# Optimization experiments

Hardware: AMD Instinct MI355X
Metric: run time of the kernel (lower is better)

## Reference

```python
import jax, jax.numpy as jnp
import numpy as np
import math

B, L, DM = 2, 2048, 1536
H, FD = 12, 16          # num_heads, feature_dim
DV = DM // H            # head_dim = 128
D2 = FD * FD            # expanded Taylor feature dim = 256
CHUNK = 128
EPS = 1e-12
LN_EPS = 1e-5


def setup_inputs() -> dict:
    key = jax.random.key(0)
    ks = jax.random.split(key, 5)
    s = lambda fan_in: 1.0 / math.sqrt(fan_in)
    return {
        "hidden_states": jax.random.normal(ks[0], (B, L, DM), jnp.float32),
        "Wq": jax.random.normal(ks[1], (DM, H * FD), jnp.float32) * s(DM),
        "Wk": jax.random.normal(ks[2], (DM, H * FD), jnp.float32) * s(DM),
        "Wv": jax.random.normal(ks[3], (DM, H * DV), jnp.float32) * s(DM),
        "Wo": jax.random.normal(ks[4], (H * DV, DM), jnp.float32) * s(H * DV),
        "ln_q_g": jnp.ones((H * FD,), jnp.float32),
        "ln_q_b": jnp.zeros((H * FD,), jnp.float32),
        "ln_k_g": jnp.ones((H * FD,), jnp.float32),
        "ln_k_b": jnp.zeros((H * FD,), jnp.float32),
    }


def _layernorm(x, g, b):
    mu = x.mean(-1, keepdims=True)
    var = ((x - mu) ** 2).mean(-1, keepdims=True)
    return (x - mu) * jax.lax.rsqrt(var + LN_EPS) * g + b


def _taylor_exp(x):
    # x: (b, h, l, d) -> flattened outer product / sqrt(d): (b, h, l, d*d)
    x2 = x[..., :, None] * x[..., None, :]
    return x2.reshape(*x.shape[:-1], -1) / math.sqrt(FD)


def _rebased_forward(hidden_states, Wq, Wk, Wv, Wo, ln_q_g, ln_q_b, ln_k_g, ln_k_b):
    b, l, _ = hidden_states.shape
    q = _layernorm(hidden_states @ Wq, ln_q_g, ln_q_b)
    k = _layernorm(hidden_states @ Wk, ln_k_g, ln_k_b)
    v = hidden_states @ Wv
    # (b, l, h*d) -> (b, h, l, d)
    q = q.reshape(b, l, H, FD).transpose(0, 2, 1, 3)
    k = k.reshape(b, l, H, FD).transpose(0, 2, 1, 3)
    v = v.reshape(b, l, H, DV).transpose(0, 2, 1, 3)
    q2 = _taylor_exp(q)  # (b, h, l, D2)
    k2 = _taylor_exp(k)

    nC = l // CHUNK
    # chunk-major layout for scan: (nC, b, h, C, .)
    q2c = q2.reshape(b, H, nC, CHUNK, D2).transpose(2, 0, 1, 3, 4)
    k2c = k2.reshape(b, H, nC, CHUNK, D2).transpose(2, 0, 1, 3, 4)
    vc = v.reshape(b, H, nC, CHUNK, DV).transpose(2, 0, 1, 3, 4)
    mask = jnp.tril(jnp.ones((CHUNK, CHUNK), q2.dtype))  # causal within chunk

    S0 = jnp.zeros((b, H, D2, DV), q2.dtype)  # running sum of k2^T v
    z0 = jnp.zeros((b, H, D2), q2.dtype)      # running sum of k2

    def step(carry, inp):
        S, z = carry
        qc, kc, vcur = inp
        A = jnp.einsum("bhcd,bhed->bhce", qc, kc) * mask  # intra-chunk scores
        num = jnp.einsum("bhcd,bhdv->bhcv", qc, S) + jnp.einsum("bhce,bhev->bhcv", A, vcur)
        den = jnp.einsum("bhcd,bhd->bhc", qc, z) + A.sum(-1)
        o = num / (den[..., None] + EPS)
        S = S + jnp.einsum("bhed,bhev->bhdv", kc, vcur)
        z = z + kc.sum(2)
        return (S, z), o

    _, o = jax.lax.scan(step, (S0, z0), (q2c, k2c, vc))
    # (nC, b, h, C, dv) -> (b, l, h*dv)
    o = o.transpose(1, 2, 0, 3, 4).reshape(b, H, l, DV).transpose(0, 2, 1, 3).reshape(b, l, H * DV)
    return o @ Wo


def reference(hidden_states, Wq, Wk, Wv, Wo, ln_q_g, ln_q_b, ln_k_g, ln_k_b):
    return _rebased_forward(hidden_states, Wq, Wk, Wv, Wo, ln_q_g, ln_q_b, ln_k_g, ln_k_b)
```

## Files before the change

kernel.cpp:

```cpp
#include <hip/hip_runtime.h>
#include <hip/hip_bf16.h>
#include <math.h>

#define Bc   2
#define Lc   2048
#define DMc  1536
#define Hc   12
#define FDc  16
#define DVc  128
#define D2c  256
#define CHK  128
#define NCH  16
#define ROWS (Bc*Lc)
#define HFD  (Hc*FDc)
#define HDV  (Hc*DVc)
#define NQK  (2*HFD)
#define NPRJ (NQK + HDV)

typedef __bf16 bf16x8 __attribute__((ext_vector_type(8)));
typedef float f32x4 __attribute__((ext_vector_type(4)));

__device__ __forceinline__ float bf2f(unsigned short u) {
    return __uint_as_float(((unsigned int)u) << 16);
}
__device__ __forceinline__ unsigned short f2bf(float v) {
    unsigned int u = __float_as_uint(v);
    unsigned int r = (u + 0x7FFFu + ((u >> 16) & 1u)) >> 16;
    return (unsigned short)r;
}
__device__ __forceinline__ unsigned int pack2(unsigned short a, unsigned short b) {
    return (unsigned int)a | ((unsigned int)b << 16);
}
__device__ __forceinline__ float ldin(const void* p, size_t i, int isf32) {
    return isf32 ? ((const float*)p)[i] : bf2f(((const unsigned short*)p)[i]);
}

#define GLL16(g, l) __builtin_amdgcn_global_load_lds( \
    (const __attribute__((address_space(1))) unsigned int*)(g), \
    (__attribute__((address_space(3))) unsigned int*)(l), 16, 0, 0)

__global__ void probe_dtype(const unsigned short* __restrict__ hs, int* __restrict__ flag) {
    const int tid = threadIdx.x;
    int sane = 0;
    for (int i = tid; i < 1024; i += 256) {
        unsigned short b = hs[2 * i];
        int e = (b >> 7) & 0xFF;
        if (e >= 97 && e <= 157) sane++;
    }
    __shared__ int tot;
    if (tid == 0) tot = 0;
    __syncthreads();
    atomicAdd(&tot, sane);
    __syncthreads();
    if (tid == 0) *flag = (tot >= 614) ? 0 : 1;
}

__global__ __launch_bounds__(256) void conv_bf16(const void* __restrict__ X,
                                                 unsigned short* __restrict__ Y,
                                                 int n4, const int* __restrict__ flagp) {
    const int f = *flagp;
    int i = blockIdx.x * 256 + threadIdx.x;
    if (i >= n4) return;
    if (f) {
        float4 x = ((const float4*)X)[i];
        ushort4 y;
        y.x = f2bf(x.x); y.y = f2bf(x.y); y.z = f2bf(x.z); y.w = f2bf(x.w);
        ((ushort4*)Y)[i] = y;
    } else {
        ((ushort4*)Y)[i] = ((const ushort4*)X)[i];
    }
}

__global__ __launch_bounds__(256) void convT_bf16(const void* __restrict__ W,
                                                  unsigned short* __restrict__ Wt,
                                                  int rows, int cols,
                                                  const int* __restrict__ flagp) {
    const int f = *flagp;
    __shared__ float tile[64][65];
    const int t = threadIdx.x;
    const int bx = blockIdx.x * 64;
    const int by = blockIdx.y * 64;
#pragma unroll
    for (int u = 0; u < 16; u++) {
        int idx = t + u * 256;
        int r = idx >> 6, c = idx & 63;
        tile[r][c] = ldin(W, (size_t)(by + r) * cols + bx + c, f);
    }
    __syncthreads();
#pragma unroll
    for (int u = 0; u < 16; u++) {
        int idx = t + u * 256;
        int r = idx >> 6, c = idx & 63;
        Wt[(size_t)(bx + r) * rows + by + c] = f2bf(tile[c][r]);
    }
}

__global__ __launch_bounds__(512) void gemm_mfma_bt(const unsigned short* __restrict__ A,
                                                    const unsigned short* __restrict__ Bt,
                                                    void* __restrict__ C,
                                                    int M, int N, int K,
                                                    int ldc,
                                                    int cMode, const int* __restrict__ flagp,
                                                    unsigned short* __restrict__ vTout) {
    const int f = *flagp;
    __shared__ __align__(16) unsigned char smem[32768];
    unsigned short* As = (unsigned short*)smem;
    unsigned short* Bsu = As + 8192;
    f32x4* scr4 = (f32x4*)smem;

    const int tid = threadIdx.x;
    const int wave = tid >> 6, lane = tid & 63;
    const int kgrp = wave >> 2;
    const int w4 = wave & 3;
    const int row0 = blockIdx.y * 128, col0 = blockIdx.x * 128;
    const int wrow = (w4 >> 1) * 64, wcol = (w4 & 1) * 64;
    const int mlane = lane & 15, quad = lane >> 4;
    const int kHalf = K >> 1;

    const unsigned short* Ab = A + (size_t)row0 * K + (size_t)kgrp * kHalf;
    const unsigned short* Bb = Bt + (size_t)col0 * K + (size_t)kgrp * kHalf;
    const int t256 = tid & 255;
    const int r0 = t256 >> 2;
    const int kc = (t256 & 3) * 8;
    const size_t off0 = (size_t)r0 * K + kc;
    const size_t off1 = (size_t)(r0 + 64) * K + kc;
    char* AsW = (char*)As + kgrp * 8192 + w4 * 1024;
    char* BsW = (char*)Bsu + kgrp * 8192 + w4 * 1024;
    const int ldsBase = kgrp * 4096;

    f32x4 acc[4][4] = {};

    for (int k0 = 0; k0 < kHalf; k0 += 32) {
        GLL16(Ab + off0 + k0, AsW);
        GLL16(Ab + off1 + k0, AsW + 4096);
        GLL16(Bb + off0 + k0, BsW);
        GLL16(Bb + off1 + k0, BsW + 4096);
        __syncthreads();
        bf16x8 a[4], b[4];
#pragma unroll
        for (int i = 0; i < 4; i++)
            a[i] = *(const bf16x8*)&As[ldsBase + (wrow + i * 16 + mlane) * 32 + quad * 8];
#pragma unroll
        for (int j = 0; j < 4; j++)
            b[j] = *(const bf16x8*)&Bsu[ldsBase + (wcol + j * 16 + mlane) * 32 + quad * 8];
#pragma unroll
        for (int i = 0; i < 4; i++)
#pragma unroll
            for (int j = 0; j < 4; j++)
                acc[i][j] = __builtin_amdgcn_mfma_f32_16x16x32_bf16(a[i], b[j], acc[i][j], 0, 0, 0);
        __syncthreads();
    }

    {
        const int col = (wave & 1) * 64 + lane;
        if (kgrp == 1 && w4 < 2) {
#pragma unroll
            for (int i = 0; i < 4; i++)
#pragma unroll
                for (int j = 0; j < 4; j++)
                    scr4[(i * 4 + j) * 128 + col] = acc[i][j];
        }
        __syncthreads();
        if (kgrp == 0 && w4 < 2) {
#pragma unroll
            for (int i = 0; i < 4; i++)
#pragma unroll
                for (int j = 0; j < 4; j++)
                    acc[i][j] += scr4[(i * 4 + j) * 128 + col];
        }
        __syncthreads();
        if (kgrp == 1 && w4 >= 2) {
#pragma unroll
            for (int i = 0; i < 4; i++)
#pragma unroll
                for (int j = 0; j < 4; j++)
                    scr4[(i * 4 + j) * 128 + col] = acc[i][j];
        }
        __syncthreads();
        if (kgrp == 0 && w4 >= 2) {
#pragma unroll
            for (int i = 0; i < 4; i++)
#pragma unroll
                for (int j = 0; j < 4; j++)
                    acc[i][j] += scr4[(i * 4 + j) * 128 + col];
        }
    }
    if (kgrp != 0) return;

    float* Cf = nullptr;
    unsigned short* Cb16 = nullptr;
    bool doT = false;
    int tOff = 0;
    if (cMode == 0) Cf = (float*)C;
    else if (cMode == 1) Cb16 = (unsigned short*)C;
    else if (cMode == 2) { if (f) Cf = (float*)C; else Cb16 = (unsigned short*)C; }
    else if (cMode == 4) {
        if (col0 < NQK) Cf = (float*)C;
        else { doT = true; tOff = NQK; }
    }
    if (cMode <= 3 && vTout) doT = true;

#pragma unroll
    for (int i = 0; i < 4; i++)
#pragma unroll
        for (int j = 0; j < 4; j++) {
            const int col = col0 + wcol + j * 16 + mlane;
            if (Cf) {
#pragma unroll
                for (int r = 0; r < 4; r++) {
                    const int row = row0 + wrow + i * 16 + quad * 4 + r;
                    Cf[(size_t)row * ldc + col] = acc[i][j][r];
                }
            } else if (Cb16) {
#pragma unroll
                for (int r = 0; r < 4; r++) {
                    const int row = row0 + wrow + i * 16 + quad * 4 + r;
                    Cb16[(size_t)row * ldc + col] = f2bf(acc[i][j][r]);
                }
            }
            if (doT) {
                ushort4 pk;
                pk.x = f2bf(acc[i][j][0]); pk.y = f2bf(acc[i][j][1]);
                pk.z = f2bf(acc[i][j][2]); pk.w = f2bf(acc[i][j][3]);
                *(ushort4*)(vTout + (size_t)(col - tOff) * M + row0 + wrow + i * 16 + quad * 4) = pk;
            }
        }
}

__global__ __launch_bounds__(192) void ln_kernel(const float* __restrict__ qk,
                                                 float* __restrict__ q, float* __restrict__ k,
                                                 const void* __restrict__ gq,
                                                 const void* __restrict__ bq,
                                                 const void* __restrict__ gk,
                                                 const void* __restrict__ bk,
                                                 const int* __restrict__ flagp) {
    const int f = *flagp;
    const int row = blockIdx.x, t = threadIdx.x;
    float vq = qk[(size_t)row * NQK + t];
    float vk = qk[(size_t)row * NQK + HFD + t];
    float s[4] = {vq, vq * vq, vk, vk * vk};
    __shared__ float part[4][3];
    const int w = t >> 6, lane = t & 63;
#pragma unroll
    for (int i = 0; i < 4; i++) {
        float v = s[i];
        for (int off = 32; off; off >>= 1) v += __shfl_down(v, off);
        if (lane == 0) part[i][w] = v;
    }
    __syncthreads();
    float sq  = part[0][0] + part[0][1] + part[0][2];
    float sq2 = part[1][0] + part[1][1] + part[1][2];
    float sk  = part[2][0] + part[2][1] + part[2][2];
    float sk2 = part[3][0] + part[3][1] + part[3][2];
    const float inv = 1.0f / (float)HFD;
    float muq = sq * inv, muk = sk * inv;
    float varq = sq2 * inv - muq * muq;
    float vark = sk2 * inv - muk * muk;
    float oq = (vq - muq) * rsqrtf(varq + 1e-5f) * ldin(gq, t, f) + ldin(bq, t, f);
    float ok = (vk - muk) * rsqrtf(vark + 1e-5f) * ldin(gk, t, f) + ldin(bk, t, f);
    q[(size_t)row * HFD + t] = oq;
    k[(size_t)row * HFD + t] = ok;
}

__global__ __launch_bounds__(256) void state_prefix_mfma(const float* __restrict__ kn,
                                                         const unsigned short* __restrict__ vT,
                                                         unsigned short* __restrict__ St,
                                                         float* __restrict__ zc) {
    const int bx = blockIdx.x;
    const int by = blockIdx.y;
    const int bh = blockIdx.z;
    const int h = bh % Hc, b = bh / Hc;
    const int t0 = bx * 16;
    const int tid = threadIdx.x;
    const int wave = tid >> 6, lane = tid & 63;
    const int mlane = lane & 15, quad = lane >> 4;

    __shared__ __align__(16) float kcs[CHK * FDc];
    __shared__ __align__(16) unsigned short K2t[16 * 136];
    __shared__ __align__(16) unsigned short Vs[64 * 136];
    __shared__ float zp[16][17];
    __shared__ float zpre[16];
    if (tid < 16) zpre[tid] = 0.f;

    f32x4 acc = {};
    const int kr = tid >> 1, khf = tid & 1;
    const int d2l = tid & 15, cg = tid >> 4;
    const int vrow = tid >> 2, vseg = tid & 3;
    const int dvL = wave * 16 + mlane;

    for (int n = 0; n < NCH; n++) {
        const int row0 = b * Lc + n * CHK;
        __syncthreads();
        {
            const float4* src = (const float4*)(kn + (size_t)(row0 + kr) * HFD + h * FDc + khf * 8);
            *(float4*)(kcs + kr * 16 + khf * 8)     = src[0];
            *(float4*)(kcs + kr * 16 + khf * 8 + 4) = src[1];
            const uint4* g = (const uint4*)(vT + (size_t)(h * 128 + by * 64 + vrow) * ROWS + row0 + vseg * 32);
            *(uint4*)(Vs + vrow * 136 + vseg * 32)      = g[0];
            *(uint4*)(Vs + vrow * 136 + vseg * 32 + 8)  = g[1];
            *(uint4*)(Vs + vrow * 136 + vseg * 32 + 16) = g[2];
            *(uint4*)(Vs + vrow * 136 + vseg * 32 + 24) = g[3];
        }
        __syncthreads();
        {
            float zs_ = 0.f;
            unsigned short pk[8];
#pragma unroll
            for (int u = 0; u < 8; u++) {
                int c = cg * 8 + u;
                float p = kcs[c * 16 + bx] * kcs[c * 16 + d2l] * 0.25f;
                zs_ += p;
                pk[u] = f2bf(p);
            }
            uint4 w;
            w.x = pack2(pk[0], pk[1]); w.y = pack2(pk[2], pk[3]);
            w.z = pack2(pk[4], pk[5]); w.w = pack2(pk[6], pk[7]);
            *(uint4*)(K2t + d2l * 136 + cg * 8) = w;
            zp[d2l][cg] = zs_;
        }
        __syncthreads();
        {
            size_t base = (((size_t)(bh * NCH + n) * 16 + bx) * 128) * 16;
            int dv = by * 64 + dvL;
            ushort4 pk;
            pk.x = f2bf(acc[0]); pk.y = f2bf(acc[1]);
            pk.z = f2bf(acc[2]); pk.w = f2bf(acc[3]);
            *(ushort4*)(St + base + (size_t)dv * 16 + quad * 4) = pk;
            if (tid < 16) {
                float s = 0.f;
#pragma unroll
                for (int c = 0; c < 16; c++) s += zp[tid][c];
                if (by == 0)
                    zc[(size_t)(bh * NCH + n) * D2c + t0 + tid] = zpre[tid];
                zpre[tid] += s;
            }
        }
        {
#pragma unroll
            for (int ks = 0; ks < 4; ks++) {
                bf16x8 a = *(const bf16x8*)(K2t + mlane * 136 + ks * 32 + quad * 8);
                bf16x8 bfr = *(const bf16x8*)(Vs + dvL * 136 + ks * 32 + quad * 8);
                acc = __builtin_amdgcn_mfma_f32_16x16x32_bf16(a, bfr, acc, 0, 0, 0);
            }
        }
    }
}

__global__ __launch_bounds__(256) void chunk_out_mfma(const float* __restrict__ qn,
                                                      const float* __restrict__ kn,
                                                      const unsigned short* __restrict__ St,
                                                      const float* __restrict__ z,
                                                      const unsigned short* __restrict__ vT,
                                                      unsigned short* __restrict__ o) {
    const int blk = blockIdx.x;
    const int n = blk & 15, bh = blk >> 4;
    const int h = bh % Hc, b = bh / Hc;
    const int row0 = b * Lc + n * CHK;
    const int tid = threadIdx.x;
    const int wave = tid >> 6, lane = tid & 63;
    const int mlane = lane & 15, quad = lane >> 4;
    const int wrow = (wave >> 1) * 64, wcol = (wave & 1) * 64;

    __shared__ __align__(16) unsigned char lds[61952];
    float* Qs   = (float*)lds;
    float* zs   = (float*)(lds + 8192);
    float* denp = (float*)(lds + 9216);
    float* dinv = (float*)(lds + 10240);
    unsigned char* U = lds + 10752;
    unsigned short* Q2s = (unsigned short*)U;
    unsigned short* Sts = (unsigned short*)(U + 10240);
    unsigned short* Kb  = (unsigned short*)U;
    unsigned short* Qb  = (unsigned short*)(U + 8192);
    unsigned short* At  = (unsigned short*)(U + 16384);
    unsigned short* Vs  = (unsigned short*)U;

    {
        int r = tid >> 1, hf = tid & 1;
        const float4* src = (const float4*)(qn + (size_t)(row0 + r) * HFD + h * FDc + hf * 8);
        *(float4*)(Qs + r * 16 + hf * 8)     = src[0];
        *(float4*)(Qs + r * 16 + hf * 8 + 4) = src[1];
        if (tid < 64)
            ((float4*)zs)[tid] = ((const float4*)(z + ((size_t)bh * NCH + n) * D2c))[tid];
    }
    __syncthreads();

    const int qc = tid >> 1, qhalf = tid & 1;
    float qr[16];
#pragma unroll
    for (int ff = 0; ff < 16; ff++) qr[ff] = Qs[qc * 16 + ff];

    f32x4 acc[4][4] = {};
    float den1 = 0.f;
    const unsigned short* Stb = St + ((size_t)bh * NCH + n) * ((size_t)D2c * DVc);

    for (int k0 = 0; k0 < 256; k0 += 32) {
        {
            unsigned short pk[16];
#pragma unroll
            for (int kk = 0; kk < 16; kk++) {
                int d2 = k0 + qhalf * 16 + kk;
                float val = qr[d2 >> 4] * qr[d2 & 15] * 0.25f;
                den1 += val * zs[d2];
                pk[kk] = f2bf(val);
            }
            uint4 w0, w1;
            w0.x = pack2(pk[0], pk[1]);  w0.y = pack2(pk[2], pk[3]);
            w0.z = pack2(pk[4], pk[5]);  w0.w = pack2(pk[6], pk[7]);
            w1.x = pack2(pk[8], pk[9]);  w1.y = pack2(pk[10], pk[11]);
            w1.z = pack2(pk[12], pk[13]); w1.w = pack2(pk[14], pk[15]);
            *(uint4*)(Q2s + qc * 40 + qhalf * 16) = w0;
            *(uint4*)(Q2s + qc * 40 + qhalf * 16 + 8) = w1;
        }
        {
            int r = tid >> 1, hf = tid & 1;
            const uint4* g = (const uint4*)(Stb + (size_t)((k0 >> 4) + hf) * 2048 + r * 16);
            uint4 d0 = g[0], d1 = g[1];
            *(uint4*)(Sts + r * 40 + hf * 16) = d0;
            *(uint4*)(Sts + r * 40 + hf * 16 + 8) = d1;
        }
        __syncthreads();
        bf16x8 a[4], bfr[4];
#pragma unroll
        for (int i = 0; i < 4; i++)
            a[i] = *(const bf16x8*)(Q2s + (wrow + i * 16 + mlane) * 40 + quad * 8);
#pragma unroll
        for (int j = 0; j < 4; j++)
            bfr[j] = *(const bf16x8*)(Sts + (wcol + j * 16 + mlane) * 40 + quad * 8);
#pragma unroll
        for (int i = 0; i < 4; i++)
#pragma unroll
            for (int j = 0; j < 4; j++)
                acc[i][j] = __builtin_amdgcn_mfma_f32_16x16x32_bf16(a[i], bfr[j], acc[i][j], 0, 0, 0);
        __syncthreads();
    }
    denp[qhalf * 128 + qc] = den1;

    {
        int r = tid >> 1, hf = tid & 1;
        if (hf == 0) {
            unsigned short pq[16], pkk[16];
#pragma unroll
            for (int ff = 0; ff < 16; ff++) pq[ff] = f2bf(Qs[r * 16 + ff]);
            const float* kg = kn + (size_t)(row0 + r) * HFD + h * FDc;
#pragma unroll
            for (int ff = 0; ff < 16; ff++) pkk[ff] = f2bf(kg[ff]);
            uint4 w;
            w.x = pack2(pq[0], pq[1]);  w.y = pack2(pq[2], pq[3]);
            w.z = pack2(pq[4], pq[5]);  w.w = pack2(pq[6], pq[7]);
            *(uint4*)(Qb + r * 32) = w;
            w.x = pack2(pq[8], pq[9]);  w.y = pack2(pq[10], pq[11]);
            w.z = pack2(pq[12], pq[13]); w.w = pack2(pq[14], pq[15]);
            *(uint4*)(Qb + r * 32 + 8) = w;
            w.x = pack2(pkk[0], pkk[1]);  w.y = pack2(pkk[2], pkk[3]);
            w.z = pack2(pkk[4], pkk[5]);  w.w = pack2(pkk[6], pkk[7]);
            *(uint4*)(Kb + r * 32) = w;
            w.x = pack2(pkk[8], pkk[9]);  w.y = pack2(pkk[10], pkk[11]);
            w.z = pack2(pkk[12], pkk[13]); w.w = pack2(pkk[14], pkk[15]);
            *(uint4*)(Kb + r * 32 + 8) = w;
        } else {
            uint4 zz = make_uint4(0, 0, 0, 0);
            *(uint4*)(Qb + r * 32 + 16) = zz;
            *(uint4*)(Qb + r * 32 + 24) = zz;
            *(uint4*)(Kb + r * 32 + 16) = zz;
            *(uint4*)(Kb + r * 32 + 24) = zz;
        }
    }
    __syncthreads();

    {
        f32x4 pacc[4][4] = {};
        bf16x8 a[4], bfr[4];
#pragma unroll
        for (int i = 0; i < 4; i++)
            a[i] = *(const bf16x8*)(Qb + (wrow + i * 16 + mlane) * 32 + quad * 8);
#pragma unroll
        for (int j = 0; j < 4; j++)
            bfr[j] = *(const bf16x8*)(Kb + (wcol + j * 16 + mlane) * 32 + quad * 8);
#pragma unroll
        for (int i = 0; i < 4; i++)
#pragma unroll
            for (int j = 0; j < 4; j++)
                pacc[i][j] = __builtin_amdgcn_mfma_f32_16x16x32_bf16(a[i], bfr[j], pacc[i][j], 0, 0, 0);
#pragma unroll
        for (int i = 0; i < 4; i++)
#pragma unroll
            for (int j = 0; j < 4; j++) {
                int e = wcol + j * 16 + mlane;
#pragma unroll
                for (int r = 0; r < 4; r++) {
                    int c = wrow + i * 16 + quad * 4 + r;
                    float p = pacc[i][j][r];
                    float aval = (e <= c) ? p * p * 0.0625f : 0.f;
                    At[c * 136 + e] = f2bf(aval);
                }
            }
    }
    __syncthreads();

    if (tid < 128) {
        float rs = 0.f;
#pragma unroll
        for (int e8 = 0; e8 < 128; e8 += 8) {
            bf16x8 v8 = *(const bf16x8*)(At + tid * 136 + e8);
#pragma unroll
            for (int u = 0; u < 8; u++) rs += (float)v8[u];
        }
        dinv[tid] = 1.0f / (denp[tid] + denp[128 + tid] + rs + 1e-12f);
    }

    for (int e0 = 0; e0 < 128; e0 += 32) {
        {
            int r = tid >> 1, hf = tid & 1;
            const uint4* g = (const uint4*)(vT + (size_t)(h * 128 + r) * ROWS + row0 + e0 + hf * 16);
            uint4 d0 = g[0], d1 = g[1];
            *(uint4*)(Vs + r * 40 + hf * 16) = d0;
            *(uint4*)(Vs + r * 40 + hf * 16 + 8) = d1;
        }
        __syncthreads();
        bf16x8 a[4], bfr[4];
#pragma unroll
        for (int i = 0; i < 4; i++)
            a[i] = *(const bf16x8*)(At + (wrow + i * 16 + mlane) * 136 + e0 + quad * 8);
#pragma unroll
        for (int j = 0; j < 4; j++)
            bfr[j] = *(const bf16x8*)(Vs + (wcol + j * 16 + mlane) * 40 + quad * 8);
#pragma unroll
        for (int i = 0; i < 4; i++)
#pragma unroll
            for (int j = 0; j < 4; j++)
                acc[i][j] = __builtin_amdgcn_mfma_f32_16x16x32_bf16(a[i], bfr[j], acc[i][j], 0, 0, 0);
        __syncthreads();
    }

#pragma unroll
    for (int i = 0; i < 4; i++)
#pragma unroll
        for (int j = 0; j < 4; j++) {
            int col = h * 128 + wcol + j * 16 + mlane;
#pragma unroll
            for (int r = 0; r < 4; r++) {
                int c = wrow + i * 16 + quad * 4 + r;
                o[(size_t)(row0 + c) * HDV + col] = f2bf(acc[i][j][r] * dinv[c]);
            }
        }
}

extern "C" void kernel_launch(void* const* d_in, const int* in_sizes, int n_in,
                              void* d_out, int out_size, void* d_ws, size_t ws_size,
                              hipStream_t stream) {
    const void* hs = d_in[0];
    const void* Wq = d_in[1];
    const void* Wk = d_in[2];
    const void* Wv = d_in[3];
    const void* Wo = d_in[4];
    const void* gq = d_in[5];
    const void* bq = d_in[6];
    const void* gk = d_in[7];
    const void* bk = d_in[8];

    int* flag = (int*)d_ws;
    float* base = (float*)d_ws + 16;
    float* qpre = base;
    float* kpre = qpre + (size_t)ROWS * HFD;
    float* vreg = kpre + (size_t)ROWS * HFD;
    float* Sc   = vreg + (size_t)ROWS * HDV;
    float* zc   = Sc + (size_t)Bc * Hc * NCH * D2c * DVc;
    float* fend = zc + (size_t)Bc * Hc * NCH * D2c;
    unsigned short* hsb = (unsigned short*)fend;
    unsigned short* ob  = hsb;
    unsigned short* Wot = hsb + (size_t)ROWS * DMc;
    unsigned short* vT  = Wot + (size_t)HDV * DMc;
    float* qk = Sc;
    unsigned short* Wqkvt = (unsigned short*)(Sc + (size_t)ROWS * NQK);
    unsigned short* St = (unsigned short*)vreg;

    probe_dtype<<<1, 256, 0, stream>>>((const unsigned short*)hs, flag);

    conv_bf16<<<(ROWS * DMc / 4 + 255) / 256, 256, 0, stream>>>(hs, hsb, ROWS * DMc / 4, flag);
    convT_bf16<<<dim3(HFD / 64, DMc / 64), 256, 0, stream>>>(Wq, Wqkvt, DMc, HFD, flag);
    convT_bf16<<<dim3(HFD / 64, DMc / 64), 256, 0, stream>>>(Wk, Wqkvt + (size_t)HFD * DMc, DMc, HFD, flag);
    convT_bf16<<<dim3(HDV / 64, DMc / 64), 256, 0, stream>>>(Wv, Wqkvt + (size_t)NQK * DMc, DMc, HDV, flag);
    convT_bf16<<<dim3(DMc / 64, HDV / 64), 256, 0, stream>>>(Wo, Wot, HDV, DMc, flag);

    gemm_mfma_bt<<<dim3(NPRJ / 128, ROWS / 128), 512, 0, stream>>>(
        hsb, Wqkvt, qk, ROWS, NPRJ, DMc, NQK, 4, flag, vT);

    ln_kernel<<<ROWS, HFD, 0, stream>>>(qk, qpre, kpre, gq, bq, gk, bk, flag);

    state_prefix_mfma<<<dim3(16, 2, Bc * Hc), 256, 0, stream>>>(kpre, vT, St, zc);

    chunk_out_mfma<<<Bc * Hc * NCH, 256, 0, stream>>>(qpre, kpre, St, zc, vT, ob);

    gemm_mfma_bt<<<dim3(DMc / 128, ROWS / 128), 512, 0, stream>>>(
        ob, Wot, d_out, ROWS, DMc, HDV, DMc, 2, flag, nullptr);
}
```

Baseline: 270.4 us.

## Double-buffer GEMM LDS tiles and split chunk_out over value-column halves

The projection GEMM now double-buffers its LDS tiles. The next K-slice is loaded while MFMAs run on the current one, which removes one barrier per iteration and hides load latency, at the cost of 64KB of LDS per block. The chunk output kernel gains a grid dimension that splits the 128 value columns into two halves. This doubles the block count to 768 for better CU occupancy, but the Q2 feature build, the intra-chunk score matrix and the denominators are now recomputed in both halves.

```diff
diff --git a/kernel.cpp b/kernel.cpp
--- a/kernel.cpp
+++ b/kernel.cpp
@@ -103,9 +103,8 @@
                                                     int cMode, const int* __restrict__ flagp,
                                                     unsigned short* __restrict__ vTout) {
     const int f = *flagp;
-    __shared__ __align__(16) unsigned char smem[32768];
-    unsigned short* As = (unsigned short*)smem;
-    unsigned short* Bsu = As + 8192;
+    __shared__ __align__(16) unsigned char smem[65536];
+    unsigned short* S16 = (unsigned short*)smem;
     f32x4* scr4 = (f32x4*)smem;
 
     const int tid = threadIdx.x;
@@ -124,31 +123,46 @@
     const int kc = (t256 & 3) * 8;
     const size_t off0 = (size_t)r0 * K + kc;
     const size_t off1 = (size_t)(r0 + 64) * K + kc;
-    char* AsW = (char*)As + kgrp * 8192 + w4 * 1024;
-    char* BsW = (char*)Bsu + kgrp * 8192 + w4 * 1024;
-    const int ldsBase = kgrp * 4096;
+    const int stA = kgrp * 8192 + w4 * 1024;
 
     f32x4 acc[4][4] = {};
-
-    for (int k0 = 0; k0 < kHalf; k0 += 32) {
-        GLL16(Ab + off0 + k0, AsW);
-        GLL16(Ab + off1 + k0, AsW + 4096);
-        GLL16(Bb + off0 + k0, BsW);
-        GLL16(Bb + off1 + k0, BsW + 4096);
-        __syncthreads();
+    const int nt = kHalf >> 5;
+
+    {
+        char* dst = (char*)smem + stA;
+        GLL16(Ab + off0, dst);
+        GLL16(Ab + off1, dst + 4096);
+        GLL16(Bb + off0, dst + 16384);
+        GLL16(Bb + off1, dst + 16384 + 4096);
+    }
+    __syncthreads();
+
+    int cur = 0;
+    for (int t = 0; t < nt; ++t) {
+        if (t + 1 < nt) {
+            const int k0n = (t + 1) << 5;
+            char* dst = (char*)smem + (cur ^ 1) * 32768 + stA;
+            GLL16(Ab + off0 + k0n, dst);
+            GLL16(Ab + off1 + k0n, dst + 4096);
+            GLL16(Bb + off0 + k0n, dst + 16384);
+            GLL16(Bb + off1 + k0n, dst + 16384 + 4096);
+        }
+        const unsigned short* Ar = S16 + cur * 16384 + kgrp * 4096;
+        const unsigned short* Br = Ar + 8192;
         bf16x8 a[4], b[4];
 #pragma unroll
         for (int i = 0; i < 4; i++)
-            a[i] = *(const bf16x8*)&As[ldsBase + (wrow + i * 16 + mlane) * 32 + quad * 8];
+            a[i] = *(const bf16x8*)&Ar[(wrow + i * 16 + mlane) * 32 + quad * 8];
 #pragma unroll
         for (int j = 0; j < 4; j++)
-            b[j] = *(const bf16x8*)&Bsu[ldsBase + (wcol + j * 16 + mlane) * 32 + quad * 8];
+            b[j] = *(const bf16x8*)&Br[(wcol + j * 16 + mlane) * 32 + quad * 8];
 #pragma unroll
         for (int i = 0; i < 4; i++)
 #pragma unroll
             for (int j = 0; j < 4; j++)
                 acc[i][j] = __builtin_amdgcn_mfma_f32_16x16x32_bf16(a[i], b[j], acc[i][j], 0, 0, 0);
         __syncthreads();
+        cur ^= 1;
     }
 
     {
@@ -352,8 +366,7 @@
                                                       const float* __restrict__ z,
                                                       const unsigned short* __restrict__ vT,
                                                       unsigned short* __restrict__ o) {
-    const int blk = blockIdx.x;
-    const int n = blk & 15, bh = blk >> 4;
+    const int n = blockIdx.x, by = blockIdx.y, bh = blockIdx.z;
     const int h = bh % Hc, b = bh / Hc;
     const int row0 = b * Lc + n * CHK;
     const int tid = threadIdx.x;
@@ -389,9 +402,11 @@
 #pragma unroll
     for (int ff = 0; ff < 16; ff++) qr[ff] = Qs[qc * 16 + ff];
 
-    f32x4 acc[4][4] = {};
+    f32x4 acc[2][4] = {};
     float den1 = 0.f;
     const unsigned short* Stb = St + ((size_t)bh * NCH + n) * ((size_t)D2c * DVc);
+    const int r2 = tid >> 2, q2i = tid & 3;
+    const int hf2 = q2i >> 1, h8 = q2i & 1;
 
     for (int k0 = 0; k0 < 256; k0 += 32) {
         {
@@ -412,22 +427,19 @@
             *(uint4*)(Q2s + qc * 40 + qhalf * 16 + 8) = w1;
         }
         {
-            int r = tid >> 1, hf = tid & 1;
-            const uint4* g = (const uint4*)(Stb + (size_t)((k0 >> 4) + hf) * 2048 + r * 16);
-            uint4 d0 = g[0], d1 = g[1];
-            *(uint4*)(Sts + r * 40 + hf * 16) = d0;
-            *(uint4*)(Sts + r * 40 + hf * 16 + 8) = d1;
-        }
-        __syncthreads();
-        bf16x8 a[4], bfr[4];
-#pragma unroll
-        for (int i = 0; i < 4; i++)
-            a[i] = *(const bf16x8*)(Q2s + (wrow + i * 16 + mlane) * 40 + quad * 8);
+            const uint4* g = (const uint4*)(Stb + (size_t)((k0 >> 4) + hf2) * 2048 + (by * 64 + r2) * 16 + h8 * 8);
+            *(uint4*)(Sts + r2 * 40 + hf2 * 16 + h8 * 8) = g[0];
+        }
+        __syncthreads();
+        bf16x8 a[2], bfr[4];
+#pragma unroll
+        for (int i = 0; i < 2; i++)
+            a[i] = *(const bf16x8*)(Q2s + (wave * 32 + i * 16 + mlane) * 40 + quad * 8);
 #pragma unroll
         for (int j = 0; j < 4; j++)
-            bfr[j] = *(const bf16x8*)(Sts + (wcol + j * 16 + mlane) * 40 + quad * 8);
-#pragma unroll
-        for (int i = 0; i < 4; i++)
+            bfr[j] = *(const bf16x8*)(Sts + (j * 16 + mlane) * 40 + quad * 8);
+#pragma unroll
+        for (int i = 0; i < 2; i++)
 #pragma unroll
             for (int j = 0; j < 4; j++)
                 acc[i][j] = __builtin_amdgcn_mfma_f32_16x16x32_bf16(a[i], bfr[j], acc[i][j], 0, 0, 0);
@@ -510,22 +522,19 @@
 
     for (int e0 = 0; e0 < 128; e0 += 32) {
         {
-            int r = tid >> 1, hf = tid & 1;
-            const uint4* g = (const uint4*)(vT + (size_t)(h * 128 + r) * ROWS + row0 + e0 + hf * 16);
-            uint4 d0 = g[0], d1 = g[1];
-            *(uint4*)(Vs + r * 40 + hf * 16) = d0;
-            *(uint4*)(Vs + r * 40 + hf * 16 + 8) = d1;
-        }
-        __syncthreads();
-        bf16x8 a[4], bfr[4];
-#pragma unroll
-        for (int i = 0; i < 4; i++)
-            a[i] = *(const bf16x8*)(At + (wrow + i * 16 + mlane) * 136 + e0 + quad * 8);
+            const uint4* g = (const uint4*)(vT + (size_t)(h * 128 + by * 64 + r2) * ROWS + row0 + e0 + hf2 * 16 + h8 * 8);
+            *(uint4*)(Vs + r2 * 40 + hf2 * 16 + h8 * 8) = g[0];
+        }
+        __syncthreads();
+        bf16x8 a[2], bfr[4];
+#pragma unroll
+        for (int i = 0; i < 2; i++)
+            a[i] = *(const bf16x8*)(At + (wave * 32 + i * 16 + mlane) * 136 + e0 + quad * 8);
 #pragma unroll
         for (int j = 0; j < 4; j++)
-            bfr[j] = *(const bf16x8*)(Vs + (wcol + j * 16 + mlane) * 40 + quad * 8);
-#pragma unroll
-        for (int i = 0; i < 4; i++)
+            bfr[j] = *(const bf16x8*)(Vs + (j * 16 + mlane) * 40 + quad * 8);
+#pragma unroll
+        for (int i = 0; i < 2; i++)
 #pragma unroll
             for (int j = 0; j < 4; j++)
                 acc[i][j] = __builtin_amdgcn_mfma_f32_16x16x32_bf16(a[i], bfr[j], acc[i][j], 0, 0, 0);
@@ -533,13 +542,13 @@
     }
 
 #pragma unroll
-    for (int i = 0; i < 4; i++)
+    for (int i = 0; i < 2; i++)
 #pragma unroll
         for (int j = 0; j < 4; j++) {
-            int col = h * 128 + wcol + j * 16 + mlane;
+            int col = h * 128 + by * 64 + j * 16 + mlane;
 #pragma unroll
             for (int r = 0; r < 4; r++) {
-                int c = wrow + i * 16 + quad * 4 + r;
+                int c = wave * 32 + i * 16 + quad * 4 + r;
                 o[(size_t)(row0 + c) * HDV + col] = f2bf(acc[i][j][r] * dinv[c]);
             }
         }
@@ -589,7 +598,7 @@
 
     state_prefix_mfma<<<dim3(16, 2, Bc * Hc), 256, 0, stream>>>(kpre, vT, St, zc);
 
-    chunk_out_mfma<<<Bc * Hc * NCH, 256, 0, stream>>>(qpre, kpre, St, zc, vT, ob);
+    chunk_out_mfma<<<dim3(NCH, 2, Bc * Hc), 256, 0, stream>>>(qpre, kpre, St, zc, vT, ob);
 
     gemm_mfma_bt<<<dim3(DMc / 128, ROWS / 128), 512, 0, stream>>>(
         ob, Wot, d_out, ROWS, DMc, HDV, DMc, 2, flag, nullptr);
```

Measured after the change: 279.7 us. 3.4% more time.
